# Kernel tuning notes

Measured on AMD Instinct MI355X. Metric: run time of the kernel, lower is better.

Reference implementation:

```python
import jax, jax.numpy as jnp
import numpy as np

B, N, D, H = 4, 512, 64, 8
DK = D // H


def setup_inputs() -> dict:
    key = jax.random.key(0)
    ks = jax.random.split(key, 9)
    s = 0.05
    return {
        "n": jax.random.normal(ks[0], (B, N, D), jnp.float32),
        "e": jax.random.normal(ks[1], (B, N, N, D), jnp.float32),
        "Wq": jax.random.normal(ks[2], (D, D), jnp.float32) * s,
        "Wk": jax.random.normal(ks[3], (D, D), jnp.float32) * s,
        "Wv": jax.random.normal(ks[4], (D, D), jnp.float32) * s,
        "Wo": jax.random.normal(ks[5], (D, D), jnp.float32) * s,
        "Wg": jax.random.normal(ks[6], (D, H), jnp.float32) * s,
        "We": jax.random.normal(ks[7], (D, H), jnp.float32) * s,
        "Oe": jax.random.normal(ks[8], (H, D), jnp.float32) * s,
    }


def reference(n, e, Wq, Wk, Wv, Wo, Wg, We, Oe):
    b, nn_, d = n.shape
    # Q,K,V: (B,H,N,DK)
    Q = (n @ Wq).reshape(b, nn_, H, DK).transpose(0, 2, 1, 3)
    K = (n @ Wk).reshape(b, nn_, H, DK).transpose(0, 2, 1, 3)
    V = (n @ Wv).reshape(b, nn_, H, DK).transpose(0, 2, 1, 3)
    # Edge bias E and gate G: (B,H,N,N)
    Eb = jnp.einsum('bqmd,dh->bhqm', e, We)
    G = jax.nn.sigmoid(jnp.einsum('bqmd,dh->bhqm', e, Wg))
    dyn_centrality = jnp.log1p(G.sum(-1))  # (B,H,N)
    # Scaled, clamped attention scores with edge bias
    A = jnp.einsum('bhqd,bhmd->bhqm', Q, K) * (DK ** -0.5)
    A = jnp.clip(A, -5.0, 5.0)
    Ehat = A + Eb
    P = jax.nn.softmax(Ehat, axis=-1)
    Vo = jnp.einsum('bhqm,bhmd->bhqd', P, V)
    Vo = Vo * dyn_centrality[..., None]
    n_out = Vo.transpose(0, 2, 1, 3).reshape(b, nn_, d) @ Wo
    e_out = jnp.einsum('bhqm,hd->bqmd', Ehat, Oe)
    return n_out, e_out
```

## Files before the change

### kernel.cpp

```cpp
#include <hip/hip_runtime.h>
#include <math.h>

#define Bn 4
#define Nn 512
#define Dn 64
#define Hn 8
#define TR 64
#define NT (Nn / TR)
#define PS 68
#define PART 80

typedef float f32x4 __attribute__((ext_vector_type(4)));

__global__ __launch_bounds__(64) void qkv_kernel(
    const float* __restrict__ nin, const float* __restrict__ Wq,
    const float* __restrict__ Wk, const float* __restrict__ Wv,
    float* __restrict__ Qw, float* __restrict__ Kw, float* __restrict__ Vw)
{
    const int row = blockIdx.x;
    const int d = threadIdx.x;
    __shared__ float nrow[Dn];
    nrow[d] = nin[row * Dn + d];
    __syncthreads();
    float aq = 0.f, ak = 0.f, av = 0.f;
#pragma unroll
    for (int k = 0; k < Dn; ++k) {
        const float nv = nrow[k];
        aq = fmaf(nv, Wq[k * Dn + d], aq);
        ak = fmaf(nv, Wk[k * Dn + d], ak);
        av = fmaf(nv, Wv[k * Dn + d], av);
    }
    Qw[row * Dn + d] = aq;
    Kw[row * Dn + d] = ak;
    Vw[row * Dn + d] = av;
}

__global__ __launch_bounds__(256, 6) void stream_kernel(
    const float* __restrict__ e,
    const float* __restrict__ Qw, const float* __restrict__ Kw,
    const float* __restrict__ Vw,
    const float* __restrict__ WeG, const float* __restrict__ WgG,
    const float* __restrict__ OeG,
    float* __restrict__ eout, float* __restrict__ part)
{
    const int bid  = blockIdx.x;
    const int bq   = bid >> 3;
    const int tile = bid & 7;
    const int b    = bq >> 9;
    const int m0   = tile * TR;
    const int t    = threadIdx.x;
    const int w    = t >> 6;
    const int l    = t & 63;

    __shared__ float e_tile[TR * Dn];
    __shared__ float ehat_s[Hn * PS];
    __shared__ __align__(16) float we_s[Hn][Dn];
    __shared__ __align__(16) float wg_s[Hn][Dn];
    __shared__ __align__(16) float oe_s[Hn][Dn];
    __shared__ float accb[4][Dn];
    __shared__ float ssb[Hn], gsb[Hn];

    float4 st[4];
    {
        const float4* ep = (const float4*)(e + ((size_t)bq * Nn + m0) * Dn);
#pragma unroll
        for (int j = 0; j < 4; ++j) st[j] = ep[j * 256 + t];
    }

    float a0, a1;
    {
        const float4* kp = (const float4*)(Kw + ((size_t)b * Nn + m0 + l) * Dn + w * 16);
        const float4 k0 = kp[0], k1 = kp[1], k2 = kp[2], k3 = kp[3];
        const float4* qp = (const float4*)(Qw + (size_t)bq * Dn + w * 16);
        const float4 q0 = qp[0], q1 = qp[1], q2 = qp[2], q3 = qp[3];
        const float qscale = 0.35355339059327373f;
        a0 = k0.x*q0.x + k0.y*q0.y + k0.z*q0.z + k0.w*q0.w
           + k1.x*q1.x + k1.y*q1.y + k1.z*q1.z + k1.w*q1.w;
        a1 = k2.x*q2.x + k2.y*q2.y + k2.z*q2.z + k2.w*q2.w
           + k3.x*q3.x + k3.y*q3.y + k3.z*q3.z + k3.w*q3.w;
        a0 = fminf(fmaxf(a0 * qscale, -5.f), 5.f);
        a1 = fminf(fmaxf(a1 * qscale, -5.f), 5.f);
    }

    for (int i = t; i < Dn * Hn; i += 256) {
        const int d = i >> 3, h = i & 7;
        we_s[h][d] = WeG[i];
        wg_s[h][d] = WgG[i];
        ((float*)oe_s)[i] = OeG[i];
    }

#pragma unroll
    for (int j = 0; j < 4; ++j) {
        const int c = j * 256 + t, r = c >> 4, g = c & 15;
        *(float4*)&e_tile[r * Dn + ((g ^ (r & 15)) << 2)] = st[j];
    }
    __syncthreads();

    float eb0 = 0.f, eb1 = 0.f, gg0 = 0.f, gg1 = 0.f;
    {
        const float4* we0 = (const float4*)we_s[2 * w];
        const float4* we1 = (const float4*)we_s[2 * w + 1];
        const float4* wg0 = (const float4*)wg_s[2 * w];
        const float4* wg1 = (const float4*)wg_s[2 * w + 1];
#pragma unroll
        for (int d4 = 0; d4 < 16; ++d4) {
            const float4 e4 = *(const float4*)&e_tile[l * Dn + (((d4 ^ (l & 15))) << 2)];
            const float4 A0 = we0[d4], A1 = we1[d4];
            const float4 G0 = wg0[d4], G1 = wg1[d4];
            eb0 = fmaf(e4.x, A0.x, fmaf(e4.y, A0.y, fmaf(e4.z, A0.z, fmaf(e4.w, A0.w, eb0))));
            eb1 = fmaf(e4.x, A1.x, fmaf(e4.y, A1.y, fmaf(e4.z, A1.z, fmaf(e4.w, A1.w, eb1))));
            gg0 = fmaf(e4.x, G0.x, fmaf(e4.y, G0.y, fmaf(e4.z, G0.z, fmaf(e4.w, G0.w, gg0))));
            gg1 = fmaf(e4.x, G1.x, fmaf(e4.y, G1.y, fmaf(e4.z, G1.z, fmaf(e4.w, G1.w, gg1))));
        }
    }

    {
        const float eh0 = a0 + eb0, eh1 = a1 + eb1;
        ehat_s[(2 * w) * PS + l]     = eh0;
        ehat_s[(2 * w + 1) * PS + l] = eh1;
        float p0 = __expf(eh0), p1 = __expf(eh1);
        float g0 = 1.f / (1.f + __expf(-gg0));
        float g1 = 1.f / (1.f + __expf(-gg1));
#pragma unroll
        for (int off = 32; off > 0; off >>= 1) {
            p0 += __shfl_xor(p0, off, 64);
            p1 += __shfl_xor(p1, off, 64);
            g0 += __shfl_xor(g0, off, 64);
            g1 += __shfl_xor(g1, off, 64);
        }
        if (l == 0) {
            ssb[2 * w] = p0; ssb[2 * w + 1] = p1;
            gsb[2 * w] = g0; gsb[2 * w + 1] = g1;
        }
    }
    __syncthreads();

    {
        float4* eo = (float4*)(eout + ((size_t)bq * Nn + m0) * Dn);
#pragma unroll
        for (int j = 0; j < 4; ++j) {
            const int c = j * 256 + t, r = c >> 4, cc = c & 15;
            f32x4 o = {0.f, 0.f, 0.f, 0.f};
#pragma unroll
            for (int h = 0; h < Hn; ++h) {
                const float ehv = ehat_s[h * PS + r];
                const float4 w4 = *(const float4*)&oe_s[h][cc * 4];
                o.x = fmaf(ehv, w4.x, o.x);
                o.y = fmaf(ehv, w4.y, o.y);
                o.z = fmaf(ehv, w4.z, o.z);
                o.w = fmaf(ehv, w4.w, o.w);
            }
            __builtin_nontemporal_store(o, (f32x4*)eo + c);
        }
    }

    {
        const int h = l >> 3;
        float acc = 0.f;
        const float* vrow = Vw + ((size_t)b * Nn + m0 + w * 16) * Dn;
#pragma unroll
        for (int i = 0; i < 16; ++i) {
            const float p = __expf(ehat_s[h * PS + w * 16 + i]);
            acc = fmaf(p, vrow[i * Dn + l], acc);
        }
        accb[w][l] = acc;
    }
    __syncthreads();

    if (w == 0) {
        const float O = accb[0][l] + accb[1][l] + accb[2][l] + accb[3][l];
        float* pb = part + (size_t)bid * PART;
        pb[l] = O;
        if (l < 8) { pb[64 + l] = ssb[l]; pb[72 + l] = gsb[l]; }
    }
}

__global__ __launch_bounds__(64) void reduce_kernel(
    const float* __restrict__ part, const float* __restrict__ WoG,
    float* __restrict__ nout)
{
    const int bq = blockIdx.x;
    const int l  = threadIdx.x;
    const int h  = l >> 3;
    const float* pb = part + (size_t)bq * NT * PART;
    float O = 0.f, S = 0.f, G = 0.f;
#pragma unroll
    for (int tl = 0; tl < NT; ++tl) {
        O += pb[tl * PART + l];
        S += pb[tl * PART + 64 + h];
        G += pb[tl * PART + 72 + h];
    }
    __shared__ float vo_s[Dn];
    vo_s[l] = (O / S) * log1pf(G);
    __syncthreads();
    float a = 0.f;
#pragma unroll
    for (int k = 0; k < Dn; ++k)
        a = fmaf(vo_s[k], WoG[k * Dn + l], a);
    nout[(size_t)bq * Dn + l] = a;
}

extern "C" void kernel_launch(void* const* d_in, const int* in_sizes, int n_in,
                              void* d_out, int out_size, void* d_ws, size_t ws_size,
                              hipStream_t stream)
{
    (void)in_sizes; (void)n_in; (void)out_size; (void)ws_size;
    const float* nin = (const float*)d_in[0];
    const float* e   = (const float*)d_in[1];
    const float* Wq  = (const float*)d_in[2];
    const float* Wk  = (const float*)d_in[3];
    const float* Wv  = (const float*)d_in[4];
    const float* Wo  = (const float*)d_in[5];
    const float* Wg  = (const float*)d_in[6];
    const float* We  = (const float*)d_in[7];
    const float* Oe  = (const float*)d_in[8];

    float* Qw   = (float*)d_ws;
    float* Kw   = Qw + Bn * Nn * Dn;
    float* Vw   = Kw + Bn * Nn * Dn;
    float* part = Vw + Bn * Nn * Dn;

    float* nout = (float*)d_out;
    float* eout = nout + Bn * Nn * Dn;

    qkv_kernel<<<Bn * Nn, 64, 0, stream>>>(nin, Wq, Wk, Wv, Qw, Kw, Vw);
    stream_kernel<<<Bn * Nn * NT, 256, 0, stream>>>(e, Qw, Kw, Vw, We, Wg, Oe,
                                                    eout, part);
    reduce_kernel<<<Bn * Nn, 64, 0, stream>>>(part, Wo, nout);
}
```

Measured before the change: 130.5 us.

## Process two edge tiles per block with register prefetch of the next tile

```diff
diff --git a/kernel.cpp b/kernel.cpp
--- a/kernel.cpp
+++ b/kernel.cpp
@@ -6,7 +6,7 @@
 #define Dn 64
 #define Hn 8
 #define TR 64
-#define NT (Nn / TR)
+#define NP 4
 #define PS 68
 #define PART 80
 
@@ -43,14 +43,13 @@
     const float* __restrict__ OeG,
     float* __restrict__ eout, float* __restrict__ part)
 {
-    const int bid  = blockIdx.x;
-    const int bq   = bid >> 3;
-    const int tile = bid & 7;
-    const int b    = bq >> 9;
-    const int m0   = tile * TR;
-    const int t    = threadIdx.x;
-    const int w    = t >> 6;
-    const int l    = t & 63;
+    const int bid = blockIdx.x;
+    const int bq  = bid >> 2;
+    const int tp  = bid & 3;
+    const int b   = bq >> 9;
+    const int t   = threadIdx.x;
+    const int w   = t >> 6;
+    const int l   = t & 63;
 
     __shared__ float e_tile[TR * Dn];
     __shared__ float ehat_s[Hn * PS];
@@ -62,24 +61,9 @@
 
     float4 st[4];
     {
-        const float4* ep = (const float4*)(e + ((size_t)bq * Nn + m0) * Dn);
+        const float4* ep = (const float4*)(e + ((size_t)bq * Nn + tp * 2 * TR) * Dn);
 #pragma unroll
         for (int j = 0; j < 4; ++j) st[j] = ep[j * 256 + t];
-    }
-
-    float a0, a1;
-    {
-        const float4* kp = (const float4*)(Kw + ((size_t)b * Nn + m0 + l) * Dn + w * 16);
-        const float4 k0 = kp[0], k1 = kp[1], k2 = kp[2], k3 = kp[3];
-        const float4* qp = (const float4*)(Qw + (size_t)bq * Dn + w * 16);
-        const float4 q0 = qp[0], q1 = qp[1], q2 = qp[2], q3 = qp[3];
-        const float qscale = 0.35355339059327373f;
-        a0 = k0.x*q0.x + k0.y*q0.y + k0.z*q0.z + k0.w*q0.w
-           + k1.x*q1.x + k1.y*q1.y + k1.z*q1.z + k1.w*q1.w;
-        a1 = k2.x*q2.x + k2.y*q2.y + k2.z*q2.z + k2.w*q2.w
-           + k3.x*q3.x + k3.y*q3.y + k3.z*q3.z + k3.w*q3.w;
-        a0 = fminf(fmaxf(a0 * qscale, -5.f), 5.f);
-        a1 = fminf(fmaxf(a1 * qscale, -5.f), 5.f);
     }
 
     for (int i = t; i < Dn * Hn; i += 256) {
@@ -89,84 +73,116 @@
         ((float*)oe_s)[i] = OeG[i];
     }
 
-#pragma unroll
-    for (int j = 0; j < 4; ++j) {
-        const int c = j * 256 + t, r = c >> 4, g = c & 15;
-        *(float4*)&e_tile[r * Dn + ((g ^ (r & 15)) << 2)] = st[j];
+    float4 q0, q1, q2, q3;
+    {
+        const float4* qp = (const float4*)(Qw + (size_t)bq * Dn + w * 16);
+        q0 = qp[0]; q1 = qp[1]; q2 = qp[2]; q3 = qp[3];
+    }
+
+    const float qscale = 0.35355339059327373f;
+    float acc = 0.f;
+    float sacc0 = 0.f, sacc1 = 0.f;
+    float gacc0 = 0.f, gacc1 = 0.f;
+
+#pragma unroll
+    for (int it = 0; it < 2; ++it) {
+        const int m0 = (tp * 2 + it) * TR;
+
+#pragma unroll
+        for (int j = 0; j < 4; ++j) {
+            const int c = j * 256 + t, r = c >> 4, g = c & 15;
+            *(float4*)&e_tile[r * Dn + ((g ^ (r & 15)) << 2)] = st[j];
+        }
+        __syncthreads();
+
+        if (it == 0) {
+            const float4* ep = (const float4*)(e + ((size_t)bq * Nn + m0 + TR) * Dn);
+#pragma unroll
+            for (int j = 0; j < 4; ++j) st[j] = ep[j * 256 + t];
+        }
+
+        const float4* kp = (const float4*)(Kw + ((size_t)b * Nn + m0 + l) * Dn + w * 16);
+        const float4 k0 = kp[0], k1 = kp[1], k2 = kp[2], k3 = kp[3];
+
+        float eb0 = 0.f, eb1 = 0.f, gg0 = 0.f, gg1 = 0.f;
+        {
+            const float4* we0 = (const float4*)we_s[2 * w];
+            const float4* we1 = (const float4*)we_s[2 * w + 1];
+            const float4* wg0 = (const float4*)wg_s[2 * w];
+            const float4* wg1 = (const float4*)wg_s[2 * w + 1];
+#pragma unroll
+            for (int d4 = 0; d4 < 16; ++d4) {
+                const float4 e4 = *(const float4*)&e_tile[l * Dn + ((d4 ^ (l & 15)) << 2)];
+                const float4 A0 = we0[d4], A1 = we1[d4];
+                const float4 G0 = wg0[d4], G1 = wg1[d4];
+                eb0 = fmaf(e4.x, A0.x, fmaf(e4.y, A0.y, fmaf(e4.z, A0.z, fmaf(e4.w, A0.w, eb0))));
+                eb1 = fmaf(e4.x, A1.x, fmaf(e4.y, A1.y, fmaf(e4.z, A1.z, fmaf(e4.w, A1.w, eb1))));
+                gg0 = fmaf(e4.x, G0.x, fmaf(e4.y, G0.y, fmaf(e4.z, G0.z, fmaf(e4.w, G0.w, gg0))));
+                gg1 = fmaf(e4.x, G1.x, fmaf(e4.y, G1.y, fmaf(e4.z, G1.z, fmaf(e4.w, G1.w, gg1))));
+            }
+        }
+
+        {
+            float a0 = k0.x*q0.x + k0.y*q0.y + k0.z*q0.z + k0.w*q0.w
+                     + k1.x*q1.x + k1.y*q1.y + k1.z*q1.z + k1.w*q1.w;
+            float a1 = k2.x*q2.x + k2.y*q2.y + k2.z*q2.z + k2.w*q2.w
+                     + k3.x*q3.x + k3.y*q3.y + k3.z*q3.z + k3.w*q3.w;
+            a0 = fminf(fmaxf(a0 * qscale, -5.f), 5.f);
+            a1 = fminf(fmaxf(a1 * qscale, -5.f), 5.f);
+            const float eh0 = a0 + eb0, eh1 = a1 + eb1;
+            ehat_s[(2 * w) * PS + l]     = eh0;
+            ehat_s[(2 * w + 1) * PS + l] = eh1;
+            float p0 = __expf(eh0), p1 = __expf(eh1);
+            float g0 = 1.f / (1.f + __expf(-gg0));
+            float g1 = 1.f / (1.f + __expf(-gg1));
+#pragma unroll
+            for (int off = 32; off > 0; off >>= 1) {
+                p0 += __shfl_xor(p0, off, 64);
+                p1 += __shfl_xor(p1, off, 64);
+                g0 += __shfl_xor(g0, off, 64);
+                g1 += __shfl_xor(g1, off, 64);
+            }
+            sacc0 += p0; sacc1 += p1;
+            gacc0 += g0; gacc1 += g1;
+        }
+        __syncthreads();
+
+        {
+            float4* eo = (float4*)(eout + ((size_t)bq * Nn + m0) * Dn);
+#pragma unroll
+            for (int j = 0; j < 4; ++j) {
+                const int c = j * 256 + t, r = c >> 4, cc = c & 15;
+                f32x4 o = {0.f, 0.f, 0.f, 0.f};
+#pragma unroll
+                for (int ho = 0; ho < Hn; ++ho) {
+                    const float ehv = ehat_s[ho * PS + r];
+                    const float4 w4 = *(const float4*)&oe_s[ho][cc * 4];
+                    o.x = fmaf(ehv, w4.x, o.x);
+                    o.y = fmaf(ehv, w4.y, o.y);
+                    o.z = fmaf(ehv, w4.z, o.z);
+                    o.w = fmaf(ehv, w4.w, o.w);
+                }
+                __builtin_nontemporal_store(o, (f32x4*)eo + c);
+            }
+        }
+
+        {
+            const int hc = l >> 3;
+            const float* vb = Vw + ((size_t)b * Nn + m0 + w * 16) * Dn;
+#pragma unroll
+            for (int i = 0; i < 16; ++i) {
+                const float p = __expf(ehat_s[hc * PS + w * 16 + i]);
+                acc = fmaf(p, vb[i * Dn + l], acc);
+            }
+        }
+    }
+
+    accb[w][l] = acc;
+    if (l == 0) {
+        ssb[2 * w] = sacc0; ssb[2 * w + 1] = sacc1;
+        gsb[2 * w] = gacc0; gsb[2 * w + 1] = gacc1;
     }
     __syncthreads();
-
-    float eb0 = 0.f, eb1 = 0.f, gg0 = 0.f, gg1 = 0.f;
-    {
-        const float4* we0 = (const float4*)we_s[2 * w];
-        const float4* we1 = (const float4*)we_s[2 * w + 1];
-        const float4* wg0 = (const float4*)wg_s[2 * w];
-        const float4* wg1 = (const float4*)wg_s[2 * w + 1];
-#pragma unroll
-        for (int d4 = 0; d4 < 16; ++d4) {
-            const float4 e4 = *(const float4*)&e_tile[l * Dn + (((d4 ^ (l & 15))) << 2)];
-            const float4 A0 = we0[d4], A1 = we1[d4];
-            const float4 G0 = wg0[d4], G1 = wg1[d4];
-            eb0 = fmaf(e4.x, A0.x, fmaf(e4.y, A0.y, fmaf(e4.z, A0.z, fmaf(e4.w, A0.w, eb0))));
-            eb1 = fmaf(e4.x, A1.x, fmaf(e4.y, A1.y, fmaf(e4.z, A1.z, fmaf(e4.w, A1.w, eb1))));
-            gg0 = fmaf(e4.x, G0.x, fmaf(e4.y, G0.y, fmaf(e4.z, G0.z, fmaf(e4.w, G0.w, gg0))));
-            gg1 = fmaf(e4.x, G1.x, fmaf(e4.y, G1.y, fmaf(e4.z, G1.z, fmaf(e4.w, G1.w, gg1))));
-        }
-    }
-
-    {
-        const float eh0 = a0 + eb0, eh1 = a1 + eb1;
-        ehat_s[(2 * w) * PS + l]     = eh0;
-        ehat_s[(2 * w + 1) * PS + l] = eh1;
-        float p0 = __expf(eh0), p1 = __expf(eh1);
-        float g0 = 1.f / (1.f + __expf(-gg0));
-        float g1 = 1.f / (1.f + __expf(-gg1));
-#pragma unroll
-        for (int off = 32; off > 0; off >>= 1) {
-            p0 += __shfl_xor(p0, off, 64);
-            p1 += __shfl_xor(p1, off, 64);
-            g0 += __shfl_xor(g0, off, 64);
-            g1 += __shfl_xor(g1, off, 64);
-        }
-        if (l == 0) {
-            ssb[2 * w] = p0; ssb[2 * w + 1] = p1;
-            gsb[2 * w] = g0; gsb[2 * w + 1] = g1;
-        }
-    }
-    __syncthreads();
-
-    {
-        float4* eo = (float4*)(eout + ((size_t)bq * Nn + m0) * Dn);
-#pragma unroll
-        for (int j = 0; j < 4; ++j) {
-            const int c = j * 256 + t, r = c >> 4, cc = c & 15;
-            f32x4 o = {0.f, 0.f, 0.f, 0.f};
-#pragma unroll
-            for (int h = 0; h < Hn; ++h) {
-                const float ehv = ehat_s[h * PS + r];
-                const float4 w4 = *(const float4*)&oe_s[h][cc * 4];
-                o.x = fmaf(ehv, w4.x, o.x);
-                o.y = fmaf(ehv, w4.y, o.y);
-                o.z = fmaf(ehv, w4.z, o.z);
-                o.w = fmaf(ehv, w4.w, o.w);
-            }
-            __builtin_nontemporal_store(o, (f32x4*)eo + c);
-        }
-    }
-
-    {
-        const int h = l >> 3;
-        float acc = 0.f;
-        const float* vrow = Vw + ((size_t)b * Nn + m0 + w * 16) * Dn;
-#pragma unroll
-        for (int i = 0; i < 16; ++i) {
-            const float p = __expf(ehat_s[h * PS + w * 16 + i]);
-            acc = fmaf(p, vrow[i * Dn + l], acc);
-        }
-        accb[w][l] = acc;
-    }
-    __syncthreads();
-
     if (w == 0) {
         const float O = accb[0][l] + accb[1][l] + accb[2][l] + accb[3][l];
         float* pb = part + (size_t)bid * PART;
@@ -182,10 +198,10 @@
     const int bq = blockIdx.x;
     const int l  = threadIdx.x;
     const int h  = l >> 3;
-    const float* pb = part + (size_t)bq * NT * PART;
+    const float* pb = part + (size_t)bq * NP * PART;
     float O = 0.f, S = 0.f, G = 0.f;
 #pragma unroll
-    for (int tl = 0; tl < NT; ++tl) {
+    for (int tl = 0; tl < NP; ++tl) {
         O += pb[tl * PART + l];
         S += pb[tl * PART + 64 + h];
         G += pb[tl * PART + 72 + h];
@@ -224,7 +240,7 @@
     float* eout = nout + Bn * Nn * Dn;
 
     qkv_kernel<<<Bn * Nn, 64, 0, stream>>>(nin, Wq, Wk, Wv, Qw, Kw, Vw);
-    stream_kernel<<<Bn * Nn * NT, 256, 0, stream>>>(e, Qw, Kw, Vw, We, Wg, Oe,
+    stream_kernel<<<Bn * Nn * NP, 256, 0, stream>>>(e, Qw, Kw, Vw, We, Wg, Oe,
                                                     eout, part);
     reduce_kernel<<<Bn * Nn, 64, 0, stream>>>(part, Wo, nout);
 }
```

New measurement: 316.1 us. 142% more time.

## Load edge tile via direct global-to-LDS DMA, keep Oe in registers, transpose ehat layout

Applied to the files above, without the earlier changes.

```diff
diff --git a/kernel.cpp b/kernel.cpp
--- a/kernel.cpp
+++ b/kernel.cpp
@@ -7,7 +7,7 @@
 #define Hn 8
 #define TR 64
 #define NT (Nn / TR)
-#define PS 68
+#define HS 12
 #define PART 80
 
 typedef float f32x4 __attribute__((ext_vector_type(4)));
@@ -53,19 +53,33 @@
     const int l    = t & 63;
 
     __shared__ float e_tile[TR * Dn];
-    __shared__ float ehat_s[Hn * PS];
+    __shared__ float ehat_s[TR * HS];
     __shared__ __align__(16) float we_s[Hn][Dn];
     __shared__ __align__(16) float wg_s[Hn][Dn];
-    __shared__ __align__(16) float oe_s[Hn][Dn];
     __shared__ float accb[4][Dn];
     __shared__ float ssb[Hn], gsb[Hn];
 
-    float4 st[4];
-    {
-        const float4* ep = (const float4*)(e + ((size_t)bq * Nn + m0) * Dn);
-#pragma unroll
-        for (int j = 0; j < 4; ++j) st[j] = ep[j * 256 + t];
-    }
+    {
+        const float* ebase = e + ((size_t)bq * Nn + m0) * Dn;
+#pragma unroll
+        for (int j = 0; j < 4; ++j) {
+            const int s = j * 256 + t;
+            const int r = s >> 4, k = s & 15;
+            const float* src = ebase + (((r << 4) | (k ^ (r & 15))) << 2);
+            unsigned int* ldst =
+                (unsigned int*)&e_tile[(j * 256 + (t & 192)) * 4];
+            __builtin_amdgcn_global_load_lds(
+                (const __attribute__((address_space(1))) unsigned int*)src,
+                (__attribute__((address_space(3))) unsigned int*)ldst,
+                16, 0, 0);
+        }
+    }
+
+    const int cc = t & 15;
+    f32x4 oev[Hn];
+#pragma unroll
+    for (int ho = 0; ho < Hn; ++ho)
+        oev[ho] = *(const f32x4*)&OeG[ho * Dn + cc * 4];
 
     float a0, a1;
     {
@@ -86,13 +100,6 @@
         const int d = i >> 3, h = i & 7;
         we_s[h][d] = WeG[i];
         wg_s[h][d] = WgG[i];
-        ((float*)oe_s)[i] = OeG[i];
-    }
-
-#pragma unroll
-    for (int j = 0; j < 4; ++j) {
-        const int c = j * 256 + t, r = c >> 4, g = c & 15;
-        *(float4*)&e_tile[r * Dn + ((g ^ (r & 15)) << 2)] = st[j];
     }
     __syncthreads();
 
@@ -104,7 +111,7 @@
         const float4* wg1 = (const float4*)wg_s[2 * w + 1];
 #pragma unroll
         for (int d4 = 0; d4 < 16; ++d4) {
-            const float4 e4 = *(const float4*)&e_tile[l * Dn + (((d4 ^ (l & 15))) << 2)];
+            const float4 e4 = *(const float4*)&e_tile[l * Dn + ((d4 ^ (l & 15)) << 2)];
             const float4 A0 = we0[d4], A1 = we1[d4];
             const float4 G0 = wg0[d4], G1 = wg1[d4];
             eb0 = fmaf(e4.x, A0.x, fmaf(e4.y, A0.y, fmaf(e4.z, A0.z, fmaf(e4.w, A0.w, eb0))));
@@ -116,8 +123,8 @@
 
     {
         const float eh0 = a0 + eb0, eh1 = a1 + eb1;
-        ehat_s[(2 * w) * PS + l]     = eh0;
-        ehat_s[(2 * w + 1) * PS + l] = eh1;
+        float2 ehp; ehp.x = eh0; ehp.y = eh1;
+        *(float2*)&ehat_s[l * HS + 2 * w] = ehp;
         float p0 = __expf(eh0), p1 = __expf(eh1);
         float g0 = 1.f / (1.f + __expf(-gg0));
         float g1 = 1.f / (1.f + __expf(-gg1));
@@ -139,28 +146,28 @@
         float4* eo = (float4*)(eout + ((size_t)bq * Nn + m0) * Dn);
 #pragma unroll
         for (int j = 0; j < 4; ++j) {
-            const int c = j * 256 + t, r = c >> 4, cc = c & 15;
-            f32x4 o = {0.f, 0.f, 0.f, 0.f};
-#pragma unroll
-            for (int h = 0; h < Hn; ++h) {
-                const float ehv = ehat_s[h * PS + r];
-                const float4 w4 = *(const float4*)&oe_s[h][cc * 4];
-                o.x = fmaf(ehv, w4.x, o.x);
-                o.y = fmaf(ehv, w4.y, o.y);
-                o.z = fmaf(ehv, w4.z, o.z);
-                o.w = fmaf(ehv, w4.w, o.w);
-            }
+            const int c = j * 256 + t, r = c >> 4;
+            const float4 ehA = *(const float4*)&ehat_s[r * HS];
+            const float4 ehB = *(const float4*)&ehat_s[r * HS + 4];
+            f32x4 o = oev[0] * ehA.x;
+            o += oev[1] * ehA.y;
+            o += oev[2] * ehA.z;
+            o += oev[3] * ehA.w;
+            o += oev[4] * ehB.x;
+            o += oev[5] * ehB.y;
+            o += oev[6] * ehB.z;
+            o += oev[7] * ehB.w;
             __builtin_nontemporal_store(o, (f32x4*)eo + c);
         }
     }
 
     {
-        const int h = l >> 3;
+        const int hc = l >> 3;
         float acc = 0.f;
         const float* vrow = Vw + ((size_t)b * Nn + m0 + w * 16) * Dn;
 #pragma unroll
         for (int i = 0; i < 16; ++i) {
-            const float p = __expf(ehat_s[h * PS + w * 16 + i]);
+            const float p = __expf(ehat_s[(w * 16 + i) * HS + hc]);
             acc = fmaf(p, vrow[i * Dn + l], acc);
         }
         accb[w][l] = acc;
@@ -224,7 +231,7 @@
     float* eout = nout + Bn * Nn * Dn;
 
     qkv_kernel<<<Bn * Nn, 64, 0, stream>>>(nin, Wq, Wk, Wv, Qw, Kw, Vw);
-    stream_kernel<<<Bn * Nn * NT, 256, 0, stream>>>(e, Qw, Kw, Vw, We, Wg, Oe,
-                                                    eout, part);
+    stream_kernel<<<Bn * Nn * NT, 256, 0, stream>>>(e, Qw, Kw, Vw, We, Wg,
+                                                    Oe, eout, part);
     reduce_kernel<<<Bn * Nn, 64, 0, stream>>>(part, Wo, nout);
 }
```

Result: slower. 183.2 us (+40.4%).
